# Performance work log

Hardware: AMD Instinct MI355X
Metric: run time of the kernel (lower is better)

## Reference

```python
import jax, jax.numpy as jnp
import numpy as np

B, TD, TE, V, D, DFF, L, H = 16, 256, 1024, 5000, 512, 2048, 6, 8

def setup_inputs():
    key = jax.random.key(0)
    ks = jax.random.split(key, 32)
    s = 0.02
    def w(k, shape):
        return jax.random.normal(k, shape, jnp.float32) * s
    # targets drawn in [3, V) so the eos filter in the torch code is a no-op
    inp = {
        "targets": jax.random.randint(ks[0], (B, TD), 3, V),
        "target_lengths": jax.random.randint(ks[1], (B,), TD // 2, TD + 1),
        "encoder_outputs": jax.random.normal(ks[2], (B, TE, D), jnp.float32),
        "encoder_output_lengths": jax.random.randint(ks[3], (B,), TE // 2, TE + 1),
        "emb": w(ks[4], (V, D)),
        "W_in": w(ks[5], (D, D)), "b_in": jnp.zeros((D,), jnp.float32),
        "ln1_g": jnp.ones((L, D), jnp.float32), "ln1_b": jnp.zeros((L, D), jnp.float32),
        "Wq1": w(ks[6], (L, D, D)), "bq1": jnp.zeros((L, D), jnp.float32),
        "Wk1": w(ks[7], (L, D, D)), "bk1": jnp.zeros((L, D), jnp.float32),
        "Wv1": w(ks[8], (L, D, D)), "bv1": jnp.zeros((L, D), jnp.float32),
        "Wo1": w(ks[9], (L, D, D)), "bo1": jnp.zeros((L, D), jnp.float32),
        "ln2_g": jnp.ones((L, D), jnp.float32), "ln2_b": jnp.zeros((L, D), jnp.float32),
        "Wq2": w(ks[10], (L, D, D)), "bq2": jnp.zeros((L, D), jnp.float32),
        "Wk2": w(ks[11], (L, D, D)), "bk2": jnp.zeros((L, D), jnp.float32),
        "Wv2": w(ks[12], (L, D, D)), "bv2": jnp.zeros((L, D), jnp.float32),
        "Wo2": w(ks[13], (L, D, D)), "bo2": jnp.zeros((L, D), jnp.float32),
        "ln3_g": jnp.ones((L, D), jnp.float32), "ln3_b": jnp.zeros((L, D), jnp.float32),
        "W_ff1": w(ks[14], (L, D, DFF)), "b_ff1": jnp.zeros((L, DFF), jnp.float32),
        "W_ff2": w(ks[15], (L, DFF, D)), "b_ff2": jnp.zeros((L, D), jnp.float32),
    }
    return inp

def _ln(x, g, b, eps=1e-5):
    m = x.mean(-1, keepdims=True)
    v = ((x - m) ** 2).mean(-1, keepdims=True)
    return (x - m) * jax.lax.rsqrt(v + eps) * g + b

def _mha(q, k, v, Wq, bq, Wk, bk, Wv, bv, Wo, bo, mask):
    Bq, Tq, Dm = q.shape
    dh = Dm // H
    def heads(x, W, bias):
        y = x @ W + bias
        return y.reshape(x.shape[0], x.shape[1], H, dh).transpose(0, 2, 1, 3)  # (B,H,T,dh)
    qh, kh, vh = heads(q, Wq, bq), heads(k, Wk, bk), heads(v, Wv, bv)
    sc = jnp.einsum('bhqd,bhkd->bhqk', qh, kh) / jnp.sqrt(jnp.float32(dh))
    sc = jnp.where(mask[:, None, :, :], jnp.float32(-1e9), sc)
    a = jax.nn.softmax(sc, axis=-1)
    ctx = jnp.einsum('bhqk,bhkd->bhqd', a, vh).transpose(0, 2, 1, 3).reshape(Bq, Tq, Dm)
    return ctx @ Wo + bo

def _pos_encoding(length, dim):
    pos = jnp.arange(length, dtype=jnp.float32)[:, None]
    div = jnp.exp(jnp.arange(0, dim, 2, dtype=jnp.float32) * (-jnp.log(jnp.float32(10000.0)) / dim))
    pe = jnp.zeros((length, dim), jnp.float32)
    pe = pe.at[:, 0::2].set(jnp.sin(pos * div)).at[:, 1::2].set(jnp.cos(pos * div))
    return pe

def _forward(targets, target_lengths, encoder_output_lengths, encoder_outputs, emb, W_in, b_in, ln1_g, ln1_b, Wq1, bq1, Wk1, bk1, Wv1, bv1, Wo1, bo1, ln2_g, ln2_b, Wq2, bq2, Wk2, bk2, Wv2, bv2, Wo2, bo2, ln3_g, ln3_b, W_ff1, b_ff1, W_ff2, b_ff2):
    Bsz, Td = targets.shape
    Te = encoder_outputs.shape[1]
    key_pad = jnp.arange(Td)[None, :] >= target_lengths[:, None]            # (B, Td) pad keys
    causal = jnp.triu(jnp.ones((Td, Td), bool), k=1)                        # subsequent mask
    self_mask = key_pad[:, None, :] | causal[None]                          # (B, Td, Td)
    enc_pad = jnp.arange(Te)[None, :] >= encoder_output_lengths[:, None]    # (B, Te)
    enc_mask = jnp.broadcast_to(enc_pad[:, None, :], (Bsz, Td, Te))
    # TransformerEmbedding: lookup * sqrt(dim), then sinusoidal PE, then input_proj
    x = emb[targets] * jnp.sqrt(jnp.float32(D)) + _pos_encoding(Td, D)[None]
    x = x @ W_in + b_in
    for l in range(L):  # pre-LN decoder layers: self-attn, cross-attn, FFN
        h = _ln(x, ln1_g[l], ln1_b[l])
        x = x + _mha(h, h, h, Wq1[l], bq1[l], Wk1[l], bk1[l], Wv1[l], bv1[l], Wo1[l], bo1[l], self_mask)
        h = _ln(x, ln2_g[l], ln2_b[l])
        x = x + _mha(h, encoder_outputs, encoder_outputs, Wq2[l], bq2[l], Wk2[l], bk2[l], Wv2[l], bv2[l], Wo2[l], bo2[l], enc_mask)
        h = _ln(x, ln3_g[l], ln3_b[l])
        x = x + (jax.nn.relu(h @ W_ff1[l] + b_ff1[l]) @ W_ff2[l] + b_ff2[l])
    # torch code stacks step_outputs[:, di, :] over di, i.e. returns the hidden states (B, Td, D)
    return x

def reference(targets, target_lengths, encoder_outputs, encoder_output_lengths, emb, W_in, b_in, ln1_g, ln1_b, Wq1, bq1, Wk1, bk1, Wv1, bv1, Wo1, bo1, ln2_g, ln2_b, Wq2, bq2, Wk2, bk2, Wv2, bv2, Wo2, bo2, ln3_g, ln3_b, W_ff1, b_ff1, W_ff2, b_ff2):
    return _forward(targets, target_lengths, encoder_output_lengths, encoder_outputs, emb, W_in, b_in, ln1_g, ln1_b, Wq1, bq1, Wk1, bk1, Wv1, bv1, Wo1, bo1, ln2_g, ln2_b, Wq2, bq2, Wk2, bk2, Wv2, bv2, Wo2, bo2, ln3_g, ln3_b, W_ff1, b_ff1, W_ff2, b_ff2)
```

## Files before the change

kernel.cpp:

```cpp
#include <hip/hip_runtime.h>
#include <hip/hip_bf16.h>

#define BB   16
#define TD   256
#define TE   1024
#define DM   512
#define DFF  2048
#define NL   6
#define NH   8
#define DH   64

typedef unsigned short u16;
typedef short short8 __attribute__((ext_vector_type(8)));
typedef float f32x4 __attribute__((ext_vector_type(4)));

__device__ __forceinline__ float b2f(u16 u) {
    unsigned int x = ((unsigned int)u) << 16;
    float f;
    __builtin_memcpy(&f, &x, 4);
    return f;
}
__device__ __forceinline__ u16 f2b(float f) {
    unsigned int x;
    __builtin_memcpy(&x, &f, 4);
    unsigned int r = x + 0x7fffu + ((x >> 16) & 1u);
    return (u16)(r >> 16);
}

__device__ __forceinline__ void gload_lds16(const u16* g, u16* l) {
    __builtin_amdgcn_global_load_lds(
        (const __attribute__((address_space(1))) unsigned int*)g,
        (__attribute__((address_space(3))) unsigned int*)l, 16, 0, 0);
}

__global__ __launch_bounds__(256) void cvt_kernel(const float* __restrict__ in,
                                                  u16* __restrict__ out, int n4) {
    int i = blockIdx.x * 256 + threadIdx.x;
    if (i < n4) {
        float4 v = reinterpret_cast<const float4*>(in)[i];
        ushort4 o;
        o.x = f2b(v.x); o.y = f2b(v.y); o.z = f2b(v.z); o.w = f2b(v.w);
        reinterpret_cast<ushort4*>(out)[i] = o;
    }
}

template <int NMAT>
struct PtrArr { const float* p[NMAT]; };

template <int NMAT>
__global__ __launch_bounds__(256) void tr_kernel(PtrArr<NMAT> P, u16* __restrict__ out,
                                                 int K, int N) {
    __shared__ u16 t[64][65];
    const float* W = P.p[blockIdx.z];
    u16* O = out + (size_t)blockIdx.z * K * N;
    int n0 = blockIdx.x * 64, k0 = blockIdx.y * 64;
    int tid = threadIdx.x;
    int r = tid >> 4, c = (tid & 15) * 4;
#pragma unroll
    for (int p = 0; p < 4; ++p) {
        int k = r + p * 16;
        float4 v = *reinterpret_cast<const float4*>(&W[(size_t)(k0 + k) * N + n0 + c]);
        t[c + 0][k] = f2b(v.x);
        t[c + 1][k] = f2b(v.y);
        t[c + 2][k] = f2b(v.z);
        t[c + 3][k] = f2b(v.w);
    }
    __syncthreads();
#pragma unroll
    for (int p = 0; p < 4; ++p) {
        int n = r + p * 16;
        ushort4 o;
        o.x = t[n][c]; o.y = t[n][c + 1]; o.z = t[n][c + 2]; o.w = t[n][c + 3];
        *reinterpret_cast<ushort4*>(&O[(size_t)(n0 + n) * K + k0 + c]) = o;
    }
}

__global__ __launch_bounds__(256) void embed_kernel(const int* __restrict__ targets,
                                                    const float* __restrict__ emb,
                                                    u16* __restrict__ out) {
    int row = blockIdx.x;
    int t   = row & (TD - 1);
    int tgt = targets[row];
    const float c = -0.017988946039015984f;
    for (int d = threadIdx.x; d < DM; d += 256) {
        float e   = emb[(size_t)tgt * DM + d] * 22.627416997969522f;
        int   i2  = d & ~1;
        float div = expf(c * (float)i2);
        float arg = (float)t * div;
        float pe  = (d & 1) ? cosf(arg) : sinf(arg);
        out[(size_t)row * DM + d] = f2b(e + pe);
    }
}

__global__ __launch_bounds__(256) void ln_kernel(const float* __restrict__ X,
                                                 const float* __restrict__ g,
                                                 const float* __restrict__ b,
                                                 size_t vo,
                                                 u16* __restrict__ O) {
    int row = blockIdx.x;
    const float* xr = X + (size_t)row * DM;
    int tid = threadIdx.x;
    float v0 = xr[tid], v1 = xr[tid + 256];
    float s = v0 + v1;
    __shared__ float red[4];
    int lane = tid & 63, wid = tid >> 6;
#pragma unroll
    for (int off = 32; off; off >>= 1) s += __shfl_xor(s, off);
    if (lane == 0) red[wid] = s;
    __syncthreads();
    float mean = (red[0] + red[1] + red[2] + red[3]) * (1.0f / 512.0f);
    float d0 = v0 - mean, d1 = v1 - mean;
    float sq = d0 * d0 + d1 * d1;
#pragma unroll
    for (int off = 32; off; off >>= 1) sq += __shfl_xor(sq, off);
    __syncthreads();
    if (lane == 0) red[wid] = sq;
    __syncthreads();
    float var = (red[0] + red[1] + red[2] + red[3]) * (1.0f / 512.0f);
    float rs  = rsqrtf(var + 1e-5f);
    O[(size_t)row * DM + tid]       = f2b(d0 * rs * g[vo + tid]       + b[vo + tid]);
    O[(size_t)row * DM + tid + 256] = f2b(d1 * rs * g[vo + tid + 256] + b[vo + tid + 256]);
}

template <int TM, int TN, bool OUTBF, bool RELU, bool RES>
__global__ __launch_bounds__(256) void gemm_bt(const u16* __restrict__ A,
                                               const u16* __restrict__ Bt,
                                               const float* __restrict__ bias, size_t bofs,
                                               const float* __restrict__ resid,
                                               void* __restrict__ C,
                                               int M, int N, int K) {
    __shared__ u16 As[2][TM * 32];
    __shared__ u16 Bs[2][TN * 32];
    int tid = threadIdx.x, wave = tid >> 6, lane = tid & 63;
    int col0 = blockIdx.x * TN, row0 = blockIdx.y * TM;
    constexpr int WM = TM / 2, WN = TN / 2;
    int wm = (wave >> 1) * WM, wn = (wave & 1) * WN;
    int lq = lane >> 4, lc = lane & 15;
    constexpr int NI = WM / 16, NJ = WN / 16;
    f32x4 acc[NI][NJ] = {};
    int srow = lane >> 2;
    int scol = (lane & 3) * 8;

    auto stage = [&](int buf, int k0) {
#pragma unroll
        for (int s = 0; s < TM / 64; ++s) {
            int rbase = wave * (TM / 4) + s * 16;
            gload_lds16(A + (size_t)(row0 + rbase + srow) * K + k0 + scol, &As[buf][rbase * 32]);
        }
#pragma unroll
        for (int s = 0; s < TN / 64; ++s) {
            int rbase = wave * (TN / 4) + s * 16;
            gload_lds16(Bt + (size_t)(col0 + rbase + srow) * K + k0 + scol, &Bs[buf][rbase * 32]);
        }
    };

    stage(0, 0);
    __syncthreads();
    int cur = 0;
    for (int k0 = 0; k0 < K; k0 += 32) {
        if (k0 + 32 < K) stage(cur ^ 1, k0 + 32);
        short8 af[NI], bf[NJ];
#pragma unroll
        for (int i = 0; i < NI; ++i)
            af[i] = *reinterpret_cast<const short8*>(&As[cur][(wm + i * 16 + lc) * 32 + lq * 8]);
#pragma unroll
        for (int j = 0; j < NJ; ++j)
            bf[j] = *reinterpret_cast<const short8*>(&Bs[cur][(wn + j * 16 + lc) * 32 + lq * 8]);
#pragma unroll
        for (int i = 0; i < NI; ++i)
#pragma unroll
            for (int j = 0; j < NJ; ++j)
                acc[i][j] = __builtin_amdgcn_mfma_f32_16x16x32_bf16(af[i], bf[j], acc[i][j], 0, 0, 0);
        __syncthreads();
        cur ^= 1;
    }

#pragma unroll
    for (int j = 0; j < NJ; ++j) {
        int n = col0 + wn + j * 16 + lc;
        float bv = bias[bofs + n];
#pragma unroll
        for (int i = 0; i < NI; ++i) {
#pragma unroll
            for (int r = 0; r < 4; ++r) {
                int m = row0 + wm + i * 16 + lq * 4 + r;
                float v = acc[i][j][r] + bv;
                if (RES)  v += resid[(size_t)m * N + n];
                if (RELU) v = fmaxf(v, 0.0f);
                if (OUTBF) ((u16*)C)[(size_t)m * N + n] = f2b(v);
                else       ((float*)C)[(size_t)m * N + n] = v;
            }
        }
    }
}

template <int NG>
struct MOut { u16* out[NG]; const float* bias[NG]; };

template <int TM, int TN, int NG>
__global__ __launch_bounds__(256) void gemm_bt_multi(const u16* __restrict__ A,
                                                     const u16* __restrict__ Bt,
                                                     MOut<NG> mo, int K) {
    __shared__ u16 As[2][TM * 32];
    __shared__ u16 Bs[2][TN * 32];
    int tid = threadIdx.x, wave = tid >> 6, lane = tid & 63;
    int col0 = blockIdx.x * TN, row0 = blockIdx.y * TM;
    constexpr int WM = TM / 2, WN = TN / 2;
    int wm = (wave >> 1) * WM, wn = (wave & 1) * WN;
    int lq = lane >> 4, lc = lane & 15;
    constexpr int NI = WM / 16, NJ = WN / 16;
    f32x4 acc[NI][NJ] = {};
    int srow = lane >> 2;
    int scol = (lane & 3) * 8;

    auto stage = [&](int buf, int k0) {
#pragma unroll
        for (int s = 0; s < TM / 64; ++s) {
            int rbase = wave * (TM / 4) + s * 16;
            gload_lds16(A + (size_t)(row0 + rbase + srow) * K + k0 + scol, &As[buf][rbase * 32]);
        }
#pragma unroll
        for (int s = 0; s < TN / 64; ++s) {
            int rbase = wave * (TN / 4) + s * 16;
            gload_lds16(Bt + (size_t)(col0 + rbase + srow) * K + k0 + scol, &Bs[buf][rbase * 32]);
        }
    };

    stage(0, 0);
    __syncthreads();
    int cur = 0;
    for (int k0 = 0; k0 < K; k0 += 32) {
        if (k0 + 32 < K) stage(cur ^ 1, k0 + 32);
        short8 af[NI], bf[NJ];
#pragma unroll
        for (int i = 0; i < NI; ++i)
            af[i] = *reinterpret_cast<const short8*>(&As[cur][(wm + i * 16 + lc) * 32 + lq * 8]);
#pragma unroll
        for (int j = 0; j < NJ; ++j)
            bf[j] = *reinterpret_cast<const short8*>(&Bs[cur][(wn + j * 16 + lc) * 32 + lq * 8]);
#pragma unroll
        for (int i = 0; i < NI; ++i)
#pragma unroll
            for (int j = 0; j < NJ; ++j)
                acc[i][j] = __builtin_amdgcn_mfma_f32_16x16x32_bf16(af[i], bf[j], acc[i][j], 0, 0, 0);
        __syncthreads();
        cur ^= 1;
    }

    int g  = col0 >> 9;
    int c0 = col0 & 511;
    u16* O = mo.out[g];
    const float* bp = mo.bias[g];
#pragma unroll
    for (int j = 0; j < NJ; ++j) {
        int n = c0 + wn + j * 16 + lc;
        float bv = bp[n];
#pragma unroll
        for (int i = 0; i < NI; ++i) {
#pragma unroll
            for (int r = 0; r < 4; ++r) {
                int m = row0 + wm + i * 16 + lq * 4 + r;
                O[(size_t)m * 512 + n] = f2b(acc[i][j][r] + bv);
            }
        }
    }
}

#define QSTR 72
#define VSTR 66

__global__ __launch_bounds__(256) void fattn_mfma(const u16* __restrict__ Q,
                                                  const u16* __restrict__ K,
                                                  const u16* __restrict__ V,
                                                  const int* __restrict__ lens,
                                                  u16* __restrict__ O,
                                                  int Tq, int Tk, int causal) {
    __shared__ u16 Qs[64 * QSTR];
    __shared__ u16 Ks[64 * QSTR];
    __shared__ u16 Ps[64 * QSTR];
    __shared__ u16 Vs[64 * VSTR];
    int tid  = threadIdx.x;
    int qt0  = blockIdx.x * 64;
    int h    = blockIdx.y;
    int b    = blockIdx.z;
    int len  = lens[b];
    int wave = tid >> 6, lane = tid & 63;
    int lq = lane >> 4, lc = lane & 15;
    int sr = tid >> 4;
    int sd = (tid & 15) * 4;

    short8 bones;
    {
        u16 v = (lc == 0) ? (u16)0x3F80 : (u16)0;
        u16 tmp[8] = { v, v, v, v, v, v, v, v };
        __builtin_memcpy(&bones, tmp, 16);
    }

#pragma unroll
    for (int i = 0; i < 4; ++i) {
        int q = sr + i * 16;
        ushort4 v = *reinterpret_cast<const ushort4*>(
            &Q[(size_t)(b * Tq + qt0 + q) * DM + h * DH + sd]);
        ushort4 w;
        w.x = f2b(b2f(v.x) * 0.125f); w.y = f2b(b2f(v.y) * 0.125f);
        w.z = f2b(b2f(v.z) * 0.125f); w.w = f2b(b2f(v.w) * 0.125f);
        *reinterpret_cast<ushort4*>(&Qs[q * QSTR + sd]) = w;
    }

    ushort4 kr[4], vr[4];
#pragma unroll
    for (int i = 0; i < 4; ++i) {
        int k = sr + i * 16;
        kr[i] = *reinterpret_cast<const ushort4*>(&K[(size_t)(b * Tk + k) * DM + h * DH + sd]);
        vr[i] = *reinterpret_cast<const ushort4*>(&V[(size_t)(b * Tk + k) * DM + h * DH + sd]);
    }
#pragma unroll
    for (int i = 0; i < 4; ++i) {
        int k = sr + i * 16;
        *reinterpret_cast<ushort4*>(&Ks[k * QSTR + sd]) = kr[i];
        Vs[(sd + 0) * VSTR + k] = vr[i].x;
        Vs[(sd + 1) * VSTR + k] = vr[i].y;
        Vs[(sd + 2) * VSTR + k] = vr[i].z;
        Vs[(sd + 3) * VSTR + k] = vr[i].w;
    }
    __syncthreads();

    short8 aq0 = *reinterpret_cast<const short8*>(&Qs[(wave * 16 + lc) * QSTR + lq * 8]);
    short8 aq1 = *reinterpret_cast<const short8*>(&Qs[(wave * 16 + lc) * QSTR + 32 + lq * 8]);

    f32x4 Ow[4] = {};
    f32x4 Ol = {};

    int kend = causal ? min(len, qt0 + 64) : len;
    for (int kt0 = 0; kt0 < kend; kt0 += 64) {
        bool more = (kt0 + 64) < kend;
        if (more) {
#pragma unroll
            for (int i = 0; i < 4; ++i) {
                int k = kt0 + 64 + sr + i * 16;
                kr[i] = *reinterpret_cast<const ushort4*>(
                    &K[(size_t)(b * Tk + k) * DM + h * DH + sd]);
                vr[i] = *reinterpret_cast<const ushort4*>(
                    &V[(size_t)(b * Tk + k) * DM + h * DH + sd]);
            }
        }

        f32x4 sa[4] = {};
#pragma unroll
        for (int n = 0; n < 4; ++n) {
            short8 bk0 = *reinterpret_cast<const short8*>(&Ks[(n * 16 + lc) * QSTR + lq * 8]);
            short8 bk1 = *reinterpret_cast<const short8*>(&Ks[(n * 16 + lc) * QSTR + 32 + lq * 8]);
            sa[n] = __builtin_amdgcn_mfma_f32_16x16x32_bf16(aq0, bk0, sa[n], 0, 0, 0);
            sa[n] = __builtin_amdgcn_mfma_f32_16x16x32_bf16(aq1, bk1, sa[n], 0, 0, 0);
        }

        int qrow_base = qt0 + wave * 16 + lq * 4;
#pragma unroll
        for (int r = 0; r < 4; ++r) {
            int qrow = qrow_base + r;
#pragma unroll
            for (int n = 0; n < 4; ++n) {
                int key = kt0 + n * 16 + lc;
                bool inv = (key >= len) || (causal && key > qrow);
                float p = inv ? 0.0f : __expf(sa[n][r] - 8.0f);
                Ps[(wave * 16 + lq * 4 + r) * QSTR + n * 16 + lc] = f2b(p);
            }
        }

        short8 ap0 = *reinterpret_cast<const short8*>(&Ps[(wave * 16 + lc) * QSTR + lq * 8]);
        short8 ap1 = *reinterpret_cast<const short8*>(&Ps[(wave * 16 + lc) * QSTR + 32 + lq * 8]);
#pragma unroll
        for (int n = 0; n < 4; ++n) {
#pragma unroll
            for (int ks = 0; ks < 2; ++ks) {
                int base = (n * 16 + lc) * VSTR + ks * 32 + lq * 8;
                const int* vp = reinterpret_cast<const int*>(&Vs[base]);
                int w[4] = { vp[0], vp[1], vp[2], vp[3] };
                short8 bv;
                __builtin_memcpy(&bv, w, 16);
                Ow[n] = __builtin_amdgcn_mfma_f32_16x16x32_bf16(ks ? ap1 : ap0, bv, Ow[n], 0, 0, 0);
            }
        }
        Ol = __builtin_amdgcn_mfma_f32_16x16x32_bf16(ap0, bones, Ol, 0, 0, 0);
        Ol = __builtin_amdgcn_mfma_f32_16x16x32_bf16(ap1, bones, Ol, 0, 0, 0);

        __syncthreads();
        if (more) {
#pragma unroll
            for (int i = 0; i < 4; ++i) {
                int k = sr + i * 16;
                *reinterpret_cast<ushort4*>(&Ks[k * QSTR + sd]) = kr[i];
                Vs[(sd + 0) * VSTR + k] = vr[i].x;
                Vs[(sd + 1) * VSTR + k] = vr[i].y;
                Vs[(sd + 2) * VSTR + k] = vr[i].z;
                Vs[(sd + 3) * VSTR + k] = vr[i].w;
            }
            __syncthreads();
        }
    }

#pragma unroll
    for (int r = 0; r < 4; ++r) {
        float lsum = __shfl(Ol[r], lane & 48);
        float inv = 1.0f / lsum;
        size_t rowoff = (size_t)(b * Tq + qt0 + wave * 16 + lq * 4 + r) * DM + h * DH;
#pragma unroll
        for (int n = 0; n < 4; ++n)
            O[rowoff + n * 16 + lc] = f2b(Ow[n][r] * inv);
    }
}

__global__ __launch_bounds__(256) void store_out_kernel(const float* __restrict__ X,
                                                        float* __restrict__ out, int n) {
    int i = blockIdx.x * 256 + threadIdx.x;
    if (i < n) out[i] = X[i];
}

extern "C" void kernel_launch(void* const* d_in, const int* in_sizes, int n_in,
                              void* d_out, int out_size, void* d_ws, size_t ws_size,
                              hipStream_t stream) {
    const int*   targets = (const int*)d_in[0];
    const int*   tlen    = (const int*)d_in[1];
    const float* enc     = (const float*)d_in[2];
    const int*   elen    = (const int*)d_in[3];
    const float* emb     = (const float*)d_in[4];
    const float* W_in    = (const float*)d_in[5];
    const float* b_in    = (const float*)d_in[6];
    const float* ln1_g   = (const float*)d_in[7];
    const float* ln1_b   = (const float*)d_in[8];
    const float* Wq1 = (const float*)d_in[9],  *bq1 = (const float*)d_in[10];
    const float* Wk1 = (const float*)d_in[11], *bk1 = (const float*)d_in[12];
    const float* Wv1 = (const float*)d_in[13], *bv1 = (const float*)d_in[14];
    const float* Wo1 = (const float*)d_in[15], *bo1 = (const float*)d_in[16];
    const float* ln2_g = (const float*)d_in[17], *ln2_b = (const float*)d_in[18];
    const float* Wq2 = (const float*)d_in[19], *bq2 = (const float*)d_in[20];
    const float* Wk2 = (const float*)d_in[21], *bk2 = (const float*)d_in[22];
    const float* Wv2 = (const float*)d_in[23], *bv2 = (const float*)d_in[24];
    const float* Wo2 = (const float*)d_in[25], *bo2 = (const float*)d_in[26];
    const float* ln3_g = (const float*)d_in[27], *ln3_b = (const float*)d_in[28];
    const float* W_ff1 = (const float*)d_in[29], *b_ff1 = (const float*)d_in[30];
    const float* W_ff2 = (const float*)d_in[31], *b_ff2 = (const float*)d_in[32];

    float* ws   = (float*)d_ws;
    float* x    = ws;
    u16*   hb   = (u16*)(ws + 2097152);
    u16*   qb   = (u16*)(ws + 3145728);
    u16*   ctx  = (u16*)(ws + 4194304);
    u16*   kb   = (u16*)(ws + 5242880);
    u16*   vb   = (u16*)(ws + 9437184);
    u16*   encb = (u16*)(ws + 13631488);
    u16*   wt_dm = (u16*)(ws + 17825792);
    u16*   wt_f1 = (u16*)(ws + 24248320);
    u16*   wt_f2 = (u16*)(ws + 27394048);
    u16*   ffh  = kb;

    PtrArr<49> pdm;
    pdm.p[0] = W_in;
    for (int l = 0; l < NL; ++l) {
        const float* ws8[8] = { Wq1, Wk1, Wv1, Wo1, Wq2, Wk2, Wv2, Wo2 };
        for (int j = 0; j < 8; ++j) pdm.p[1 + l * 8 + j] = ws8[j] + (size_t)l * DM * DM;
    }
    PtrArr<6> pf1, pf2;
    for (int l = 0; l < NL; ++l) {
        pf1.p[l] = W_ff1 + (size_t)l * DM * DFF;
        pf2.p[l] = W_ff2 + (size_t)l * DFF * DM;
    }
    tr_kernel<49><<<dim3(8, 8, 49), 256, 0, stream>>>(pdm, wt_dm, 512, 512);
    tr_kernel<6><<<dim3(32, 8, 6), 256, 0, stream>>>(pf1, wt_f1, 512, 2048);
    tr_kernel<6><<<dim3(8, 32, 6), 256, 0, stream>>>(pf2, wt_f2, 2048, 512);

    const size_t WDM = (size_t)512 * 512;
    const size_t WFF = (size_t)512 * 2048;

    const dim3 gdm(8, 64);
    const dim3 gqkv(24, 64);
    const dim3 gkv2(8, 128);
    const dim3 gf1(16, 32);
    const dim3 gattn(TD / 64, NH, BB);

    cvt_kernel<<<8192, 256, 0, stream>>>(enc, encb, BB * TE * DM / 4);
    embed_kernel<<<4096, 256, 0, stream>>>(targets, emb, hb);
    gemm_bt<64, 64, false, false, false><<<gdm, 256, 0, stream>>>(hb, wt_dm, b_in, 0, nullptr, x, 4096, 512, 512);

    for (int l = 0; l < NL; ++l) {
        const size_t vo = (size_t)l * DM;
        const size_t fv = (size_t)l * DFF;
        const u16* tq1 = wt_dm + (1 + l * 8 + 0) * WDM;
        const u16* to1 = wt_dm + (1 + l * 8 + 3) * WDM;
        const u16* tq2 = wt_dm + (1 + l * 8 + 4) * WDM;
        const u16* tk2 = wt_dm + (1 + l * 8 + 5) * WDM;
        const u16* to2 = wt_dm + (1 + l * 8 + 7) * WDM;
        const u16* tf1 = wt_f1 + l * WFF;
        const u16* tf2 = wt_f2 + l * WFF;

        ln_kernel<<<4096, 256, 0, stream>>>(x, ln1_g, ln1_b, vo, hb);
        {
            MOut<3> mo;
            mo.out[0] = qb; mo.out[1] = kb; mo.out[2] = vb;
            mo.bias[0] = bq1 + vo; mo.bias[1] = bk1 + vo; mo.bias[2] = bv1 + vo;
            gemm_bt_multi<64, 64, 3><<<gqkv, 256, 0, stream>>>(hb, tq1, mo, 512);
        }
        fattn_mfma<<<gattn, 256, 0, stream>>>(qb, kb, vb, tlen, ctx, TD, TD, 1);
        gemm_bt<64, 64, false, false, true><<<gdm, 256, 0, stream>>>(ctx, to1, bo1, vo, x, x, 4096, 512, 512);

        ln_kernel<<<4096, 256, 0, stream>>>(x, ln2_g, ln2_b, vo, hb);
        gemm_bt<64, 64, true, false, false><<<gdm, 256, 0, stream>>>(hb, tq2, bq2, vo, nullptr, qb, 4096, 512, 512);
        {
            MOut<2> mo;
            mo.out[0] = kb; mo.out[1] = vb;
            mo.bias[0] = bk2 + vo; mo.bias[1] = bv2 + vo;
            gemm_bt_multi<128, 128, 2><<<gkv2, 256, 0, stream>>>(encb, tk2, mo, 512);
        }
        fattn_mfma<<<gattn, 256, 0, stream>>>(qb, kb, vb, elen, ctx, TD, TE, 0);
        gemm_bt<64, 64, false, false, true><<<gdm, 256, 0, stream>>>(ctx, to2, bo2, vo, x, x, 4096, 512, 512);

        ln_kernel<<<4096, 256, 0, stream>>>(x, ln3_g, ln3_b, vo, hb);
        gemm_bt<128, 128, true, true, false><<<gf1, 256, 0, stream>>>(hb, tf1, b_ff1, fv, nullptr, ffh, 4096, 2048, 512);
        gemm_bt<64, 64, false, false, true><<<gdm, 256, 0, stream>>>(ffh, tf2, b_ff2, vo, x, x, 4096, 512, 2048);
    }

    store_out_kernel<<<8192, 256, 0, stream>>>(x, (float*)d_out, BB * TD * DM);
}
```

Before: 1.361 ms.

## Triple-buffer GEMM K-loop with vmcnt waits and skip masked encoder KV tiles

Both GEMM kernels move from a double-buffered LDS pipeline with __syncthreads to a three-stage ring that keeps two tile loads in flight. Explicit s_waitcnt vmcnt(N) plus a raw barrier lets the newest prefetch stay outstanding while older data is consumed, hiding more global latency. The cross-attention K/V projection also returns early for row tiles beyond each batch's encoder length (rounded up to 64), skipping work for padded positions. This relies on the attention kernel never reading those unwritten rows, and the extra LDS buffer lowers occupancy.

After: 1.431 ms. +5.1%, slower.

```diff
diff --git a/kernel.cpp b/kernel.cpp
--- a/kernel.cpp
+++ b/kernel.cpp
@@ -31,6 +31,18 @@
     __builtin_amdgcn_global_load_lds(
         (const __attribute__((address_space(1))) unsigned int*)g,
         (__attribute__((address_space(3))) unsigned int*)l, 16, 0, 0);
+}
+
+template <int L>
+__device__ __forceinline__ void wait_vm_pipe(bool keep) {
+    if (keep) {
+        if constexpr (L == 2)      asm volatile("s_waitcnt vmcnt(2)" ::: "memory");
+        else if constexpr (L == 3) asm volatile("s_waitcnt vmcnt(3)" ::: "memory");
+        else if constexpr (L == 4) asm volatile("s_waitcnt vmcnt(4)" ::: "memory");
+        else                       asm volatile("s_waitcnt vmcnt(0)" ::: "memory");
+    } else {
+        asm volatile("s_waitcnt vmcnt(0)" ::: "memory");
+    }
 }
 
 __global__ __launch_bounds__(256) void cvt_kernel(const float* __restrict__ in,
@@ -129,11 +141,12 @@
                                                const float* __restrict__ resid,
                                                void* __restrict__ C,
                                                int M, int N, int K) {
-    __shared__ u16 As[2][TM * 32];
-    __shared__ u16 Bs[2][TN * 32];
+    __shared__ u16 As[3][TM * 32];
+    __shared__ u16 Bs[3][TN * 32];
     int tid = threadIdx.x, wave = tid >> 6, lane = tid & 63;
     int col0 = blockIdx.x * TN, row0 = blockIdx.y * TM;
     constexpr int WM = TM / 2, WN = TN / 2;
+    constexpr int L = TM / 64 + TN / 64;
     int wm = (wave >> 1) * WM, wn = (wave & 1) * WN;
     int lq = lane >> 4, lc = lane & 15;
     constexpr int NI = WM / 16, NJ = WN / 16;
@@ -154,11 +167,16 @@
         }
     };
 
+    int nk = K >> 5;
     stage(0, 0);
-    __syncthreads();
-    int cur = 0;
-    for (int k0 = 0; k0 < K; k0 += 32) {
-        if (k0 + 32 < K) stage(cur ^ 1, k0 + 32);
+    if (nk > 1) stage(1, 32);
+    wait_vm_pipe<L>(nk > 1);
+    __builtin_amdgcn_s_barrier();
+
+    for (int k = 0; k < nk; ++k) {
+        bool more2 = (k + 2) < nk;
+        if (more2) stage((k + 2) % 3, (k + 2) * 32);
+        int cur = k % 3;
         short8 af[NI], bf[NJ];
 #pragma unroll
         for (int i = 0; i < NI; ++i)
@@ -171,8 +189,10 @@
 #pragma unroll
             for (int j = 0; j < NJ; ++j)
                 acc[i][j] = __builtin_amdgcn_mfma_f32_16x16x32_bf16(af[i], bf[j], acc[i][j], 0, 0, 0);
-        __syncthreads();
-        cur ^= 1;
+        if (k + 1 < nk) {
+            wait_vm_pipe<L>(more2);
+            __builtin_amdgcn_s_barrier();
+        }
     }
 
 #pragma unroll
@@ -200,12 +220,23 @@
 template <int TM, int TN, int NG>
 __global__ __launch_bounds__(256) void gemm_bt_multi(const u16* __restrict__ A,
                                                      const u16* __restrict__ Bt,
-                                                     MOut<NG> mo, int K) {
-    __shared__ u16 As[2][TM * 32];
-    __shared__ u16 Bs[2][TN * 32];
+                                                     MOut<NG> mo, int K,
+                                                     const int* __restrict__ lens,
+                                                     int rbShift) {
+    __shared__ u16 As[3][TM * 32];
+    __shared__ u16 Bs[3][TN * 32];
     int tid = threadIdx.x, wave = tid >> 6, lane = tid & 63;
     int col0 = blockIdx.x * TN, row0 = blockIdx.y * TM;
+
+    if (lens) {
+        int bb  = row0 >> rbShift;
+        int rl  = row0 & ((1 << rbShift) - 1);
+        int lim = (lens[bb] + 63) & ~63;
+        if (rl >= lim) return;
+    }
+
     constexpr int WM = TM / 2, WN = TN / 2;
+    constexpr int L = TM / 64 + TN / 64;
     int wm = (wave >> 1) * WM, wn = (wave & 1) * WN;
     int lq = lane >> 4, lc = lane & 15;
     constexpr int NI = WM / 16, NJ = WN / 16;
@@ -226,11 +257,16 @@
         }
     };
 
+    int nk = K >> 5;
     stage(0, 0);
-    __syncthreads();
-    int cur = 0;
-    for (int k0 = 0; k0 < K; k0 += 32) {
-        if (k0 + 32 < K) stage(cur ^ 1, k0 + 32);
+    if (nk > 1) stage(1, 32);
+    wait_vm_pipe<L>(nk > 1);
+    __builtin_amdgcn_s_barrier();
+
+    for (int k = 0; k < nk; ++k) {
+        bool more2 = (k + 2) < nk;
+        if (more2) stage((k + 2) % 3, (k + 2) * 32);
+        int cur = k % 3;
         short8 af[NI], bf[NJ];
 #pragma unroll
         for (int i = 0; i < NI; ++i)
@@ -243,8 +279,10 @@
 #pragma unroll
             for (int j = 0; j < NJ; ++j)
                 acc[i][j] = __builtin_amdgcn_mfma_f32_16x16x32_bf16(af[i], bf[j], acc[i][j], 0, 0, 0);
-        __syncthreads();
-        cur ^= 1;
+        if (k + 1 < nk) {
+            wait_vm_pipe<L>(more2);
+            __builtin_amdgcn_s_barrier();
+        }
     }
 
     int g  = col0 >> 9;
@@ -498,7 +536,7 @@
             MOut<3> mo;
             mo.out[0] = qb; mo.out[1] = kb; mo.out[2] = vb;
             mo.bias[0] = bq1 + vo; mo.bias[1] = bk1 + vo; mo.bias[2] = bv1 + vo;
-            gemm_bt_multi<64, 64, 3><<<gqkv, 256, 0, stream>>>(hb, tq1, mo, 512);
+            gemm_bt_multi<64, 64, 3><<<gqkv, 256, 0, stream>>>(hb, tq1, mo, 512, nullptr, 0);
         }
         fattn_mfma<<<gattn, 256, 0, stream>>>(qb, kb, vb, tlen, ctx, TD, TD, 1);
         gemm_bt<64, 64, false, false, true><<<gdm, 256, 0, stream>>>(ctx, to1, bo1, vo, x, x, 4096, 512, 512);
@@ -509,7 +547,7 @@
             MOut<2> mo;
             mo.out[0] = kb; mo.out[1] = vb;
             mo.bias[0] = bk2 + vo; mo.bias[1] = bv2 + vo;
-            gemm_bt_multi<128, 128, 2><<<gkv2, 256, 0, stream>>>(encb, tk2, mo, 512);
+            gemm_bt_multi<128, 128, 2><<<gkv2, 256, 0, stream>>>(encb, tk2, mo, 512, elen, 10);
         }
         fattn_mfma<<<gattn, 256, 0, stream>>>(qb, kb, vb, elen, ctx, TD, TE, 0);
         gemm_bt<64, 64, false, false, true><<<gdm, 256, 0, stream>>>(ctx, to2, bo2, vo, x, x, 4096, 512, 512);
```
